# Kernel optimization log

Measured on AMD Instinct MI355X. Metric: run time of the kernel, lower is better.

Reference implementation:

```python
import jax, jax.numpy as jnp
import numpy as np

EMB, HEADS = 1024, 16
B, T = 4, 1024

def setup_inputs() -> dict:
    key = jax.random.key(0)
    ks = jax.random.split(key, 6)
    sc = 1.0 / np.sqrt(EMB)
    return {
        "x": jax.random.normal(ks[0], (B, T, EMB), jnp.float32),
        "Wq": jax.random.normal(ks[1], (EMB, EMB), jnp.float32) * sc,
        "Wk": jax.random.normal(ks[2], (EMB, EMB), jnp.float32) * sc,
        "Wv": jax.random.normal(ks[3], (EMB, EMB), jnp.float32) * sc,
        "Wo": jax.random.normal(ks[4], (EMB, EMB), jnp.float32) * sc,
        "bo": jnp.zeros((EMB,), jnp.float32),
    }

def reference(x, Wq, Wk, Wv, Wo, bo):
    b, t, e = x.shape
    h = HEADS
    s = e // h
    # nn.Linear(emb, emb, bias=False): y = x @ W.T
    q = (x @ Wq.T).reshape(b, t, h, s).transpose(0, 2, 1, 3)  # (b,h,t,s)
    k = (x @ Wk.T).reshape(b, t, h, s).transpose(0, 2, 1, 3)
    v = (x @ Wv.T).reshape(b, t, h, s).transpose(0, 2, 1, 3)
    scale = e ** 0.25  # original scales q and k each by emb**(1/4)
    q = q / scale
    k = k / scale
    dot = jnp.einsum('bhqs,bhks->bhqk', q, k)  # (b,h,t,t)
    # causal mask: strict upper triangle -> -inf (mask_diagonal=False)
    causal = jnp.tril(jnp.ones((t, t), dtype=bool))
    dot = jnp.where(causal[None, None], dot, -jnp.inf)
    attn = jax.nn.softmax(dot, axis=-1)
    out = jnp.einsum('bhqk,bhks->bhqs', attn, v)  # (b,h,t,s)
    out = out.transpose(0, 2, 1, 3).reshape(b, t, e)
    return out @ Wo.T + bo
```

## Files before the change

### kernel.cpp

```cpp
#include <hip/hip_runtime.h>
#include <hip/hip_bf16.h>
#include <stdint.h>


typedef __attribute__((ext_vector_type(8))) short short8;
typedef __attribute__((ext_vector_type(4))) float f32x4;
typedef __attribute__((ext_vector_type(16))) float f32x16;

__device__ __forceinline__ unsigned short f2bf(float f) {
    union { float f; unsigned int u; } v; v.f = f;
    unsigned int r = v.u + 0x7FFFu + ((v.u >> 16) & 1u);
    return (unsigned short)(r >> 16);
}
__device__ __forceinline__ unsigned short f2bf_trunc(float f) {
    union { float f; unsigned int u; } v; v.f = f;
    return (unsigned short)(v.u >> 16);
}

__device__ __forceinline__ void gload_lds16(const ushort* g, ushort* l) {
    __builtin_amdgcn_global_load_lds(
        (const __attribute__((address_space(1))) void*)g,
        (__attribute__((address_space(3))) void*)l,
        16, 0, 0);
}

__device__ __forceinline__ void wait_vmcnt_0() { asm volatile("s_waitcnt vmcnt(0)" ::: "memory"); }
__device__ __forceinline__ void wait_vmcnt_3() { asm volatile("s_waitcnt vmcnt(3)" ::: "memory"); }
__device__ __forceinline__ void wait_vmcnt_4() { asm volatile("s_waitcnt vmcnt(4)" ::: "memory"); }

__device__ __forceinline__ void block_barrier() {
    __builtin_amdgcn_sched_barrier(0);
    __builtin_amdgcn_s_barrier();
    __builtin_amdgcn_sched_barrier(0);
}
__device__ __forceinline__ void lgk0() {
    asm volatile("s_waitcnt lgkmcnt(0)" ::: "memory");
    __builtin_amdgcn_sched_barrier(0);
}

__global__ __launch_bounds__(256) void cast_bf16(
    const float* __restrict__ x,  const float* __restrict__ wq,
    const float* __restrict__ wk, const float* __restrict__ wv,
    const float* __restrict__ wo, ushort* __restrict__ dst)
{
    size_t e0 = (size_t)(blockIdx.x * 256 + threadIdx.x) * 4;
    const float* src; size_t off;
    if      (e0 < 4194304u) { src = x;  off = e0; }
    else if (e0 < 5242880u) { src = wq; off = e0 - 4194304u; }
    else if (e0 < 6291456u) { src = wk; off = e0 - 5242880u; }
    else if (e0 < 7340032u) { src = wv; off = e0 - 6291456u; }
    else                    { src = wo; off = e0 - 7340032u; }
    float4 v = *(const float4*)(src + off);
    ushort4 o;
    o.x = f2bf(v.x); o.y = f2bf(v.y); o.z = f2bf(v.z); o.w = f2bf(v.w);
    *(ushort4*)(dst + e0) = o;
}

__global__ __launch_bounds__(512) void gemm_qkv_8ph(
    const ushort* __restrict__ A, const ushort* __restrict__ B,
    ushort* __restrict__ Qb, ushort* __restrict__ Kb, ushort* __restrict__ Vtb)
{
    __shared__ ushort lds[2][2][2][128 * 64];

    const int id = blockIdx.x;
    const int swz = (id & 7) * 24 + (id >> 3);
    const int bx = swz % 12, by = swz / 12;
    const int n0 = bx * 256, m0 = by * 256;
    const int t = threadIdx.x, w = t >> 6, l = t & 63;
    const int l15 = l & 15, l4 = l >> 4;
    const int wr = w >> 2, wc = w & 3;
    const int K = 1024;

    auto stage_half = [&](const ushort* gsrc, ushort* dst) {
        #pragma unroll
        for (int i = 0; i < 2; ++i) {
            int slot = i * 512 + t;
            int r = slot >> 3, blk = slot & 7;
            gload_lds16(gsrc + (size_t)r * K + ((blk ^ (r & 7)) << 3),
                        dst + (i * 512 + w * 64) * 8);
        }
    };
    auto stageA = [&](int kt, int h, int buf) {
        stage_half(A + (size_t)(m0 + h * 128) * K + kt * 64, &lds[buf][0][h][0]);
    };
    auto stageB = [&](int kt, int h, int buf) {
        stage_half(B + (size_t)(n0 + h * 128) * K + kt * 64, &lds[buf][1][h][0]);
    };

    short8 af[8];
    short8 vb0[4], vb1[4];
    f32x4 acc[8][4] = {};

    auto readA = [&](int buf, int qm) {
        const ushort* base = &lds[buf][0][wr][0];
        #pragma unroll
        for (int kk = 0; kk < 2; ++kk)
            #pragma unroll
            for (int mt = 0; mt < 4; ++mt) {
                int row = qm * 64 + mt * 16 + l15;
                af[kk * 4 + mt] = *(const short8*)
                    &base[row * 64 + (((kk * 4 + l4) ^ (row & 7)) << 3)];
            }
    };
    auto readB0 = [&](int buf, int qn) {
        const ushort* base = &lds[buf][1][wc >> 1][0];
        #pragma unroll
        for (int kk = 0; kk < 2; ++kk)
            #pragma unroll
            for (int nt = 0; nt < 2; ++nt) {
                int row = (wc & 1) * 64 + qn * 32 + nt * 16 + l15;
                vb0[kk * 2 + nt] = *(const short8*)
                    &base[row * 64 + (((kk * 4 + l4) ^ (row & 7)) << 3)];
            }
    };
    auto readB1 = [&](int buf, int qn) {
        const ushort* base = &lds[buf][1][wc >> 1][0];
        #pragma unroll
        for (int kk = 0; kk < 2; ++kk)
            #pragma unroll
            for (int nt = 0; nt < 2; ++nt) {
                int row = (wc & 1) * 64 + qn * 32 + nt * 16 + l15;
                vb1[kk * 2 + nt] = *(const short8*)
                    &base[row * 64 + (((kk * 4 + l4) ^ (row & 7)) << 3)];
            }
    };
    auto mfma_vb0 = [&](int qm, int qn) {
        __builtin_amdgcn_s_setprio(1);
        #pragma unroll
        for (int kk = 0; kk < 2; ++kk)
            #pragma unroll
            for (int mt = 0; mt < 4; ++mt)
                #pragma unroll
                for (int nt = 0; nt < 2; ++nt)
                    acc[qm * 4 + mt][qn * 2 + nt] =
                        __builtin_amdgcn_mfma_f32_16x16x32_bf16(
                            af[kk * 4 + mt], vb0[kk * 2 + nt],
                            acc[qm * 4 + mt][qn * 2 + nt], 0, 0, 0);
        __builtin_amdgcn_s_setprio(0);
    };
    auto mfma_vb1 = [&](int qm, int qn) {
        __builtin_amdgcn_s_setprio(1);
        #pragma unroll
        for (int kk = 0; kk < 2; ++kk)
            #pragma unroll
            for (int mt = 0; mt < 4; ++mt)
                #pragma unroll
                for (int nt = 0; nt < 2; ++nt)
                    acc[qm * 4 + mt][qn * 2 + nt] =
                        __builtin_amdgcn_mfma_f32_16x16x32_bf16(
                            af[kk * 4 + mt], vb1[kk * 2 + nt],
                            acc[qm * 4 + mt][qn * 2 + nt], 0, 0, 0);
        __builtin_amdgcn_s_setprio(0);
    };

    stageB(0, 0, 0); stageB(0, 1, 0); stageA(0, 0, 0); stageA(0, 1, 0);
    stageB(1, 0, 1); stageB(1, 1, 1);
    wait_vmcnt_4();
    block_barrier();

    for (int j = 0; j < 8; ++j) {
        const bool more = (j < 7);
        readA(0, 0); readB0(0, 0);
        stageA(2 * j + 1, 0, 1);
        block_barrier(); lgk0();
        mfma_vb0(0, 0);
        block_barrier();
        readB1(0, 1);
        stageA(2 * j + 1, 1, 1);
        block_barrier(); lgk0();
        mfma_vb1(0, 1);
        block_barrier();
        readA(0, 1);
        if (more) stageB(2 * j + 2, 0, 0);
        block_barrier(); lgk0();
        mfma_vb1(1, 1);
        block_barrier();
        if (more) stageB(2 * j + 2, 1, 0);
        block_barrier(); lgk0();
        mfma_vb0(1, 0);
        if (more) wait_vmcnt_4(); else wait_vmcnt_0();
        block_barrier();
        readA(1, 0); readB0(1, 0);
        if (more) stageA(2 * j + 2, 0, 0);
        block_barrier(); lgk0();
        mfma_vb0(0, 0);
        block_barrier();
        readB1(1, 1);
        if (more) stageA(2 * j + 2, 1, 0);
        block_barrier(); lgk0();
        mfma_vb1(0, 1);
        block_barrier();
        readA(1, 1);
        if (more) stageB(2 * j + 3, 0, 1);
        block_barrier(); lgk0();
        mfma_vb1(1, 1);
        block_barrier();
        if (more) stageB(2 * j + 3, 1, 1);
        block_barrier(); lgk0();
        mfma_vb0(1, 0);
        if (more) { wait_vmcnt_4(); block_barrier(); }
    }

    #pragma unroll
    for (int qm = 0; qm < 2; ++qm) {
        #pragma unroll
        for (int mt = 0; mt < 4; ++mt) {
            int row = m0 + wr * 128 + qm * 64 + mt * 16 + l4 * 4;
            int b = row >> 10, tq = row & 1023;
            #pragma unroll
            for (int qn = 0; qn < 2; ++qn) {
                #pragma unroll
                for (int nt = 0; nt < 2; ++nt) {
                    int col = n0 + wc * 64 + qn * 32 + nt * 16 + l15;
                    int sel = col >> 10;
                    int cw  = col & 1023;
                    int h = cw >> 6, s = cw & 63;
                    f32x4 v = acc[qm * 4 + mt][qn * 2 + nt];
                    if (sel == 2) {
                        ushort4 o;
                        o.x = f2bf(v[0]); o.y = f2bf(v[1]);
                        o.z = f2bf(v[2]); o.w = f2bf(v[3]);
                        *(ushort4*)&Vtb[(((size_t)(b * 16 + h)) * 64 + s) * 1024 + tq] = o;
                    } else {
                        ushort* dst = (sel == 0) ? Qb : Kb;
                        float scl = (sel == 0) ? 0.03125f : 1.0f;
                        #pragma unroll
                        for (int jj = 0; jj < 4; ++jj)
                            dst[(((size_t)(b * 16 + h)) * 1024 + tq + jj) * 64 + s] =
                                f2bf(v[jj] * scl);
                    }
                }
            }
        }
    }
}

template<int MODE, int BM, int WRg, int WCg>
__global__ __launch_bounds__(256) void gemm_bt(
    const ushort* __restrict__ A, const ushort* __restrict__ B,
    float* __restrict__ Cout, const float* __restrict__ bias)
{
    constexpr int MF = BM / (32 * WRg);
    constexpr int NF = 128 / (32 * WCg);
    constexpr int NSTEP = 32;
    const int K = 1024;
    const int n0 = blockIdx.x * 128;
    const int m0 = blockIdx.y * BM;
    const int t  = threadIdx.x;
    const int w  = t >> 6, l = t & 63;
    const int l31 = l & 31, lh = l >> 5;
    const int wr = w / WCg, wc = w % WCg;

    __shared__ ushort As[3 * BM * 32];
    __shared__ ushort Bs[3 * 128 * 32];

    auto stage = [&](int j) {
        const int buf = j % 3;
        const int k0 = j * 32;
        #pragma unroll
        for (int i = 0; i < BM / 64; ++i) {
            int slot = i * 256 + t;
            int r = slot >> 2, blk = slot & 3;
            gload_lds16(A + (size_t)(m0 + r) * K + k0 + ((blk ^ ((r >> 1) & 3)) << 3),
                        &As[buf * BM * 32 + (i * 256 + w * 64) * 8]);
        }
        #pragma unroll
        for (int i = 0; i < 2; ++i) {
            int slot = i * 256 + t;
            int r = slot >> 2, blk = slot & 3;
            gload_lds16(B + (size_t)(n0 + r) * K + k0 + ((blk ^ ((r >> 1) & 3)) << 3),
                        &Bs[buf * 128 * 32 + (i * 256 + w * 64) * 8]);
        }
    };

    f32x16 acc[MF][NF] = {};

    stage(0); stage(1);
    for (int kt = 0; kt < NSTEP; ++kt) {
        if (kt < NSTEP - 1) { if (BM == 128) wait_vmcnt_4(); else wait_vmcnt_3(); }
        else wait_vmcnt_0();
        block_barrier();
        if (kt + 2 < NSTEP) stage(kt + 2);

        const ushort* Ab = &As[(kt % 3) * BM * 32];
        const ushort* Bb = &Bs[(kt % 3) * 128 * 32];
        #pragma unroll
        for (int kk = 0; kk < 2; ++kk) {
            const int c = kk * 2 + lh;
            short8 af[MF], bf[NF];
            #pragma unroll
            for (int mt = 0; mt < MF; ++mt) {
                int row = wr * (MF * 32) + mt * 32 + l31;
                af[mt] = *(const short8*)&Ab[row * 32 + ((c ^ ((row >> 1) & 3)) << 3)];
            }
            #pragma unroll
            for (int nt = 0; nt < NF; ++nt) {
                int row = wc * (NF * 32) + nt * 32 + l31;
                bf[nt] = *(const short8*)&Bs[(kt % 3) * 128 * 32 + row * 32 + ((c ^ ((row >> 1) & 3)) << 3)];
            }
            #pragma unroll
            for (int mt = 0; mt < MF; ++mt)
                #pragma unroll
                for (int nt = 0; nt < NF; ++nt)
                    acc[mt][nt] = __builtin_amdgcn_mfma_f32_32x32x16_bf16(
                        af[mt], bf[nt], acc[mt][nt], 0, 0, 0);
        }
    }

    #pragma unroll
    for (int mt = 0; mt < MF; ++mt) {
        int rbase = m0 + wr * (MF * 32) + mt * 32 + 4 * lh;
        #pragma unroll
        for (int nt = 0; nt < NF; ++nt) {
            int col = n0 + wc * (NF * 32) + nt * 32 + l31;
            float bi = bias[col];
            #pragma unroll
            for (int reg = 0; reg < 16; ++reg) {
                int row = rbase + (reg & 3) + 8 * (reg >> 2);
                Cout[(size_t)row * 1024 + col] = acc[mt][nt][reg] + bi;
            }
        }
    }
}

__global__ __launch_bounds__(64) void attn_kernel(
    const ushort* __restrict__ Q, const ushort* __restrict__ Kp,
    const ushort* __restrict__ Vt, ushort* __restrict__ O)
{
    __shared__ ushort Ps[32 * 64];
    const int id = blockIdx.x;
    const int bh = id & 63;
    const int g  = 31 - (id >> 6);
    const int l = threadIdx.x;
    const int l15 = l & 15, l4 = l >> 4;

    const ushort* Qbase = Q  + ((size_t)bh * 1024 + (size_t)g * 32) * 64;
    const ushort* Kbase = Kp + (size_t)bh * 1024 * 64;
    const ushort* Vtb   = Vt + (size_t)bh * 64 * 1024;

    short8 qa[2][2];
    #pragma unroll
    for (int kk = 0; kk < 2; ++kk)
        #pragma unroll
        for (int mt = 0; mt < 2; ++mt)
            qa[kk][mt] = *(const short8*)(Qbase + (size_t)(mt * 16 + l15) * 64 + (kk * 4 + l4) * 8);

    float l_acc[8];
    #pragma unroll
    for (int i = 0; i < 8; ++i) l_acc[i] = 0.f;
    f32x4 accO[2][4] = {};

    const int qmin = g * 32;
    const int nkv = (g >> 1) + 1;
    for (int kvt = 0; kvt < nkv; ++kvt) {
        short8 kb[2][4];
        #pragma unroll
        for (int kk = 0; kk < 2; ++kk)
            #pragma unroll
            for (int nt = 0; nt < 4; ++nt)
                kb[kk][nt] = *(const short8*)
                    (Kbase + (size_t)(kvt * 64 + nt * 16 + l15) * 64 + (kk * 4 + l4) * 8);
        short8 vb[2][4];
        #pragma unroll
        for (int kk = 0; kk < 2; ++kk)
            #pragma unroll
            for (int st = 0; st < 4; ++st)
                vb[kk][st] = *(const short8*)
                    (Vtb + (size_t)(st * 16 + l15) * 1024 + kvt * 64 + (kk * 4 + l4) * 8);

        f32x4 sf[2][4] = {};
        #pragma unroll
        for (int kk = 0; kk < 2; ++kk)
            #pragma unroll
            for (int mt = 0; mt < 2; ++mt)
                #pragma unroll
                for (int nt = 0; nt < 4; ++nt)
                    sf[mt][nt] = __builtin_amdgcn_mfma_f32_16x16x32_bf16(
                        qa[kk][mt], kb[kk][nt], sf[mt][nt], 0, 0, 0);

        const bool domask = (kvt * 64 + 63 > qmin);
        #pragma unroll
        for (int mt = 0; mt < 2; ++mt) {
            #pragma unroll
            for (int r = 0; r < 4; ++r) {
                const int qrow = qmin + mt * 16 + l4 * 4 + r;
                const int qlocal = mt * 16 + l4 * 4 + r;
                const int idx = mt * 4 + r;
                #pragma unroll
                for (int nt = 0; nt < 4; ++nt) {
                    int col = kvt * 64 + nt * 16 + l15;
                    float p = (domask && col > qrow) ? 0.f : __expf(sf[mt][nt][r]);
                    l_acc[idx] += p;
                    int c = nt * 16 + l15;
                    Ps[qlocal * 64 + (((c >> 3) ^ (qlocal & 7)) << 3) + (c & 7)] =
                        f2bf_trunc(p);
                }
            }
        }
        lgk0();

        #pragma unroll
        for (int kk = 0; kk < 2; ++kk) {
            short8 pa[2];
            #pragma unroll
            for (int mt = 0; mt < 2; ++mt) {
                int row = mt * 16 + l15;
                pa[mt] = *(const short8*)&Ps[row * 64 + (((kk * 4 + l4) ^ (row & 7)) << 3)];
            }
            #pragma unroll
            for (int mt = 0; mt < 2; ++mt)
                #pragma unroll
                for (int st = 0; st < 4; ++st)
                    accO[mt][st] = __builtin_amdgcn_mfma_f32_16x16x32_bf16(
                        pa[mt], vb[kk][st], accO[mt][st], 0, 0, 0);
        }
    }

    const int b = bh >> 4, h = bh & 15;
    #pragma unroll
    for (int mt = 0; mt < 2; ++mt) {
        #pragma unroll
        for (int r = 0; r < 4; ++r) {
            float s = l_acc[mt * 4 + r];
            s += __shfl_xor(s, 1);
            s += __shfl_xor(s, 2);
            s += __shfl_xor(s, 4);
            s += __shfl_xor(s, 8);
            float inv = 1.0f / s;
            int tq = qmin + mt * 16 + l4 * 4 + r;
            #pragma unroll
            for (int st = 0; st < 4; ++st) {
                int sc = st * 16 + l15;
                O[((size_t)b * 1024 + tq) * 1024 + h * 64 + sc] =
                    f2bf(accO[mt][st][r] * inv);
            }
        }
    }
}

extern "C" void kernel_launch(void* const* d_in, const int* in_sizes, int n_in,
                              void* d_out, int out_size, void* d_ws, size_t ws_size,
                              hipStream_t stream) {
    const float* x  = (const float*)d_in[0];
    const float* wq = (const float*)d_in[1];
    const float* wk = (const float*)d_in[2];
    const float* wv = (const float*)d_in[3];
    const float* wo = (const float*)d_in[4];
    const float* bo = (const float*)d_in[5];
    float* out = (float*)d_out;

    ushort* ws  = (ushort*)d_ws;
    ushort* xb  = ws;
    ushort* wb  = ws + (4u << 20);
    ushort* Qb  = ws + (8u << 20);
    ushort* Kb  = ws + (12u << 20);
    ushort* Vtb = ws + (16u << 20);
    ushort* Ob  = ws + (20u << 20);

    cast_bf16<<<8192, 256, 0, stream>>>(x, wq, wk, wv, wo, ws);
    gemm_qkv_8ph<<<192, 512, 0, stream>>>(xb, wb, Qb, Kb, Vtb);
    attn_kernel<<<2048, 64, 0, stream>>>(Qb, Kb, Vtb, Ob);
    gemm_bt<1, 64, 1, 4><<<dim3(8, 64), 256, 0, stream>>>(
        Ob, wb + (3u << 20), out, bo);
}
```

Baseline: 106.1 us.

## Split attention KV loop across two wavefronts and combine partial results in LDS

The attention kernel now runs two wavefronts per block. Each wavefront processes half of the causal KV tiles for the same 32-query tile, and wave 1's partial output and row sums are reduced into wave 0 through shared memory. No running max is kept, so the two partials can be added directly. This is a split-K flash-decoding style change meant to shorten the per-block critical path and raise parallelism. In exchange it adds LDS usage (about 8KB plus 2×4KB), a block barrier and a combine step. It also includes a trivial cleanup that reuses the Bb pointer in the GEMM.

```diff
diff --git a/kernel.cpp b/kernel.cpp
--- a/kernel.cpp
+++ b/kernel.cpp
@@ -296,7 +296,7 @@
             #pragma unroll
             for (int nt = 0; nt < NF; ++nt) {
                 int row = wc * (NF * 32) + nt * 32 + l31;
-                bf[nt] = *(const short8*)&Bs[(kt % 3) * 128 * 32 + row * 32 + ((c ^ ((row >> 1) & 3)) << 3)];
+                bf[nt] = *(const short8*)&Bb[row * 32 + ((c ^ ((row >> 1) & 3)) << 3)];
             }
             #pragma unroll
             for (int mt = 0; mt < MF; ++mt)
@@ -323,15 +323,18 @@
     }
 }
 
-__global__ __launch_bounds__(64) void attn_kernel(
+__global__ __launch_bounds__(128) void attn_kernel(
     const ushort* __restrict__ Q, const ushort* __restrict__ Kp,
     const ushort* __restrict__ Vt, ushort* __restrict__ O)
 {
-    __shared__ ushort Ps[32 * 64];
+    __shared__ ushort Ps[2][32 * 64];
+    __shared__ float cmb[32 * 64];
+    __shared__ float lcmb[32];
+
     const int id = blockIdx.x;
     const int bh = id & 63;
     const int g  = 31 - (id >> 6);
-    const int l = threadIdx.x;
+    const int t = threadIdx.x, w = t >> 6, l = t & 63;
     const int l15 = l & 15, l4 = l >> 4;
 
     const ushort* Qbase = Q  + ((size_t)bh * 1024 + (size_t)g * 32) * 64;
@@ -352,15 +355,18 @@
 
     const int qmin = g * 32;
     const int nkv = (g >> 1) + 1;
-    for (int kvt = 0; kvt < nkv; ++kvt) {
-        short8 kb[2][4];
+    const int h = (nkv + 1) >> 1;
+    const int kv_lo = w ? h : 0;
+    const int kv_hi = w ? nkv : h;
+
+    for (int kvt = kv_lo; kvt < kv_hi; ++kvt) {
+        short8 kb[2][4], vb[2][4];
         #pragma unroll
         for (int kk = 0; kk < 2; ++kk)
             #pragma unroll
             for (int nt = 0; nt < 4; ++nt)
                 kb[kk][nt] = *(const short8*)
                     (Kbase + (size_t)(kvt * 64 + nt * 16 + l15) * 64 + (kk * 4 + l4) * 8);
-        short8 vb[2][4];
         #pragma unroll
         for (int kk = 0; kk < 2; ++kk)
             #pragma unroll
@@ -392,7 +398,7 @@
                     float p = (domask && col > qrow) ? 0.f : __expf(sf[mt][nt][r]);
                     l_acc[idx] += p;
                     int c = nt * 16 + l15;
-                    Ps[qlocal * 64 + (((c >> 3) ^ (qlocal & 7)) << 3) + (c & 7)] =
+                    Ps[w][qlocal * 64 + (((c >> 3) ^ (qlocal & 7)) << 3) + (c & 7)] =
                         f2bf_trunc(p);
                 }
             }
@@ -405,7 +411,7 @@
             #pragma unroll
             for (int mt = 0; mt < 2; ++mt) {
                 int row = mt * 16 + l15;
-                pa[mt] = *(const short8*)&Ps[row * 64 + (((kk * 4 + l4) ^ (row & 7)) << 3)];
+                pa[mt] = *(const short8*)&Ps[w][row * 64 + (((kk * 4 + l4) ^ (row & 7)) << 3)];
             }
             #pragma unroll
             for (int mt = 0; mt < 2; ++mt)
@@ -416,23 +422,47 @@
         }
     }
 
-    const int b = bh >> 4, h = bh & 15;
+    float lred[8];
     #pragma unroll
-    for (int mt = 0; mt < 2; ++mt) {
-        #pragma unroll
-        for (int r = 0; r < 4; ++r) {
-            float s = l_acc[mt * 4 + r];
-            s += __shfl_xor(s, 1);
-            s += __shfl_xor(s, 2);
-            s += __shfl_xor(s, 4);
-            s += __shfl_xor(s, 8);
-            float inv = 1.0f / s;
-            int tq = qmin + mt * 16 + l4 * 4 + r;
-            #pragma unroll
-            for (int st = 0; st < 4; ++st) {
-                int sc = st * 16 + l15;
-                O[((size_t)b * 1024 + tq) * 1024 + h * 64 + sc] =
-                    f2bf(accO[mt][st][r] * inv);
+    for (int i = 0; i < 8; ++i) {
+        float s = l_acc[i];
+        s += __shfl_xor(s, 1);
+        s += __shfl_xor(s, 2);
+        s += __shfl_xor(s, 4);
+        s += __shfl_xor(s, 8);
+        lred[i] = s;
+    }
+
+    if (w == 1) {
+        #pragma unroll
+        for (int mt = 0; mt < 2; ++mt) {
+            #pragma unroll
+            for (int r = 0; r < 4; ++r) {
+                int row = mt * 16 + l4 * 4 + r;
+                if (l15 == 0) lcmb[row] = lred[mt * 4 + r];
+                #pragma unroll
+                for (int st = 0; st < 4; ++st)
+                    cmb[row * 64 + st * 16 + l15] = accO[mt][st][r];
+            }
+        }
+    }
+    __syncthreads();
+    if (w == 0) {
+        const int b = bh >> 4, hh = bh & 15;
+        #pragma unroll
+        for (int mt = 0; mt < 2; ++mt) {
+            #pragma unroll
+            for (int r = 0; r < 4; ++r) {
+                int row = mt * 16 + l4 * 4 + r;
+                float s = lred[mt * 4 + r] + lcmb[row];
+                float inv = 1.0f / s;
+                int tq = qmin + row;
+                #pragma unroll
+                for (int st = 0; st < 4; ++st) {
+                    int sc = st * 16 + l15;
+                    float o = accO[mt][st][r] + cmb[row * 64 + sc];
+                    O[((size_t)b * 1024 + tq) * 1024 + hh * 64 + sc] = f2bf(o * inv);
+                }
             }
         }
     }
@@ -459,7 +489,7 @@
 
     cast_bf16<<<8192, 256, 0, stream>>>(x, wq, wk, wv, wo, ws);
     gemm_qkv_8ph<<<192, 512, 0, stream>>>(xb, wb, Qb, Kb, Vtb);
-    attn_kernel<<<2048, 64, 0, stream>>>(Qb, Kb, Vtb, Ob);
+    attn_kernel<<<2048, 128, 0, stream>>>(Qb, Kb, Vtb, Ob);
     gemm_bt<1, 64, 1, 4><<<dim3(8, 64), 256, 0, stream>>>(
         Ob, wb + (3u << 20), out, bo);
 }
```

Result: no change. 105.3 us (-0.7%).

## Keep attention probabilities in registers via transposed 32x32 MFMA and permlane swap

Applied to the files above, without the earlier changes.

The attention kernel now computes S^T = K·Q^T with 32x32x16 MFMAs, so each lane holds the scores for one query row. The probabilities are packed to bf16 with v_cvt_pk_bf16_f32 and rearranged with v_permlane32_swap into the A-operand layout for the PV MFMA. This removes the LDS round trip and the wait on it, and it also simplifies the row-sum reduction. The causal tail is peeled out so masking and the upper half-tile are done only where needed, at the cost of higher register pressure and reliance on gfx950-specific instructions.

```diff
diff --git a/kernel.cpp b/kernel.cpp
--- a/kernel.cpp
+++ b/kernel.cpp
@@ -11,10 +11,6 @@
     union { float f; unsigned int u; } v; v.f = f;
     unsigned int r = v.u + 0x7FFFu + ((v.u >> 16) & 1u);
     return (unsigned short)(r >> 16);
-}
-__device__ __forceinline__ unsigned short f2bf_trunc(float f) {
-    union { float f; unsigned int u; } v; v.f = f;
-    return (unsigned short)(v.u >> 16);
 }
 
 __device__ __forceinline__ void gload_lds16(const ushort* g, ushort* l) {
@@ -36,6 +32,15 @@
 __device__ __forceinline__ void lgk0() {
     asm volatile("s_waitcnt lgkmcnt(0)" ::: "memory");
     __builtin_amdgcn_sched_barrier(0);
+}
+
+__device__ __forceinline__ unsigned int cvtpk(float lo, float hi) {
+    unsigned int r;
+    asm("v_cvt_pk_bf16_f32 %0, %1, %2" : "=v"(r) : "v"(lo), "v"(hi));
+    return r;
+}
+__device__ __forceinline__ void plswap(unsigned int& x, unsigned int& y) {
+    asm volatile("v_permlane32_swap_b32 %0, %1" : "+v"(x), "+v"(y));
 }
 
 __global__ __launch_bounds__(256) void cast_bf16(
@@ -296,7 +301,7 @@
             #pragma unroll
             for (int nt = 0; nt < NF; ++nt) {
                 int row = wc * (NF * 32) + nt * 32 + l31;
-                bf[nt] = *(const short8*)&Bs[(kt % 3) * 128 * 32 + row * 32 + ((c ^ ((row >> 1) & 3)) << 3)];
+                bf[nt] = *(const short8*)&Bb[row * 32 + ((c ^ ((row >> 1) & 3)) << 3)];
             }
             #pragma unroll
             for (int mt = 0; mt < MF; ++mt)
@@ -327,114 +332,126 @@
     const ushort* __restrict__ Q, const ushort* __restrict__ Kp,
     const ushort* __restrict__ Vt, ushort* __restrict__ O)
 {
-    __shared__ ushort Ps[32 * 64];
     const int id = blockIdx.x;
     const int bh = id & 63;
     const int g  = 31 - (id >> 6);
     const int l = threadIdx.x;
-    const int l15 = l & 15, l4 = l >> 4;
+    const int l31 = l & 31, hi = l >> 5;
 
     const ushort* Qbase = Q  + ((size_t)bh * 1024 + (size_t)g * 32) * 64;
     const ushort* Kbase = Kp + (size_t)bh * 1024 * 64;
     const ushort* Vtb   = Vt + (size_t)bh * 64 * 1024;
 
-    short8 qa[2][2];
+    short8 qb[4];
     #pragma unroll
-    for (int kk = 0; kk < 2; ++kk)
-        #pragma unroll
-        for (int mt = 0; mt < 2; ++mt)
-            qa[kk][mt] = *(const short8*)(Qbase + (size_t)(mt * 16 + l15) * 64 + (kk * 4 + l4) * 8);
-
-    float l_acc[8];
-    #pragma unroll
-    for (int i = 0; i < 8; ++i) l_acc[i] = 0.f;
-    f32x4 accO[2][4] = {};
-
-    const int qmin = g * 32;
+    for (int ks = 0; ks < 4; ++ks)
+        qb[ks] = *(const short8*)(Qbase + (size_t)l31 * 64 + ks * 16 + hi * 8);
+
+    f32x16 accO0 = {}, accO1 = {};
+    float lsum = 0.f;
+    const int qrow = g * 32 + l31;
     const int nkv = (g >> 1) + 1;
-    for (int kvt = 0; kvt < nkv; ++kvt) {
-        short8 kb[2][4];
-        #pragma unroll
-        for (int kk = 0; kk < 2; ++kk)
-            #pragma unroll
-            for (int nt = 0; nt < 4; ++nt)
-                kb[kk][nt] = *(const short8*)
-                    (Kbase + (size_t)(kvt * 64 + nt * 16 + l15) * 64 + (kk * 4 + l4) * 8);
-        short8 vb[2][4];
-        #pragma unroll
-        for (int kk = 0; kk < 2; ++kk)
-            #pragma unroll
-            for (int st = 0; st < 4; ++st)
-                vb[kk][st] = *(const short8*)
-                    (Vtb + (size_t)(st * 16 + l15) * 1024 + kvt * 64 + (kk * 4 + l4) * 8);
-
-        f32x4 sf[2][4] = {};
-        #pragma unroll
-        for (int kk = 0; kk < 2; ++kk)
-            #pragma unroll
-            for (int mt = 0; mt < 2; ++mt)
-                #pragma unroll
-                for (int nt = 0; nt < 4; ++nt)
-                    sf[mt][nt] = __builtin_amdgcn_mfma_f32_16x16x32_bf16(
-                        qa[kk][mt], kb[kk][nt], sf[mt][nt], 0, 0, 0);
-
-        const bool domask = (kvt * 64 + 63 > qmin);
-        #pragma unroll
-        for (int mt = 0; mt < 2; ++mt) {
-            #pragma unroll
-            for (int r = 0; r < 4; ++r) {
-                const int qrow = qmin + mt * 16 + l4 * 4 + r;
-                const int qlocal = mt * 16 + l4 * 4 + r;
-                const int idx = mt * 4 + r;
-                #pragma unroll
-                for (int nt = 0; nt < 4; ++nt) {
-                    int col = kvt * 64 + nt * 16 + l15;
-                    float p = (domask && col > qrow) ? 0.f : __expf(sf[mt][nt][r]);
-                    l_acc[idx] += p;
-                    int c = nt * 16 + l15;
-                    Ps[qlocal * 64 + (((c >> 3) ^ (qlocal & 7)) << 3) + (c & 7)] =
-                        f2bf_trunc(p);
-                }
-            }
-        }
-        lgk0();
-
-        #pragma unroll
-        for (int kk = 0; kk < 2; ++kk) {
-            short8 pa[2];
-            #pragma unroll
-            for (int mt = 0; mt < 2; ++mt) {
-                int row = mt * 16 + l15;
-                pa[mt] = *(const short8*)&Ps[row * 64 + (((kk * 4 + l4) ^ (row & 7)) << 3)];
-            }
-            #pragma unroll
-            for (int mt = 0; mt < 2; ++mt)
-                #pragma unroll
-                for (int st = 0; st < 4; ++st)
-                    accO[mt][st] = __builtin_amdgcn_mfma_f32_16x16x32_bf16(
-                        pa[mt], vb[kk][st], accO[mt][st], 0, 0, 0);
-        }
-    }
-
+
+    auto pv_ks = [&](const float* pf, int ks, const short8* vb0p, const short8* vb1p) {
+        const int r0 = (ks & 1) * 8;
+        unsigned int A0 = cvtpk(pf[r0 + 0], pf[r0 + 1]);
+        unsigned int A1 = cvtpk(pf[r0 + 2], pf[r0 + 3]);
+        unsigned int B0 = cvtpk(pf[r0 + 4], pf[r0 + 5]);
+        unsigned int B1 = cvtpk(pf[r0 + 6], pf[r0 + 7]);
+        plswap(A0, B0);
+        plswap(A1, B1);
+        union { unsigned int u[4]; short8 s; } pa;
+        pa.u[0] = A0; pa.u[1] = A1; pa.u[2] = B0; pa.u[3] = B1;
+        accO0 = __builtin_amdgcn_mfma_f32_32x32x16_bf16(pa.s, vb0p[ks], accO0, 0, 0, 0);
+        accO1 = __builtin_amdgcn_mfma_f32_32x32x16_bf16(pa.s, vb1p[ks], accO1, 0, 0, 0);
+    };
+
+    for (int kvt = 0; kvt < nkv - 1; ++kvt) {
+        short8 ka0[4], ka1[4], vb0[4], vb1[4];
+        #pragma unroll
+        for (int ks = 0; ks < 4; ++ks) {
+            ka0[ks] = *(const short8*)(Kbase + (size_t)(kvt * 64 + l31) * 64 + ks * 16 + hi * 8);
+            ka1[ks] = *(const short8*)(Kbase + (size_t)(kvt * 64 + 32 + l31) * 64 + ks * 16 + hi * 8);
+        }
+        #pragma unroll
+        for (int ks = 0; ks < 4; ++ks) {
+            vb0[ks] = *(const short8*)(Vtb + (size_t)l31 * 1024 + kvt * 64 + ks * 16 + hi * 8);
+            vb1[ks] = *(const short8*)(Vtb + (size_t)(32 + l31) * 1024 + kvt * 64 + ks * 16 + hi * 8);
+        }
+        f32x16 sf0 = {}, sf1 = {};
+        #pragma unroll
+        for (int ks = 0; ks < 4; ++ks) {
+            sf0 = __builtin_amdgcn_mfma_f32_32x32x16_bf16(ka0[ks], qb[ks], sf0, 0, 0, 0);
+            sf1 = __builtin_amdgcn_mfma_f32_32x32x16_bf16(ka1[ks], qb[ks], sf1, 0, 0, 0);
+        }
+        float p[32];
+        #pragma unroll
+        for (int r = 0; r < 16; ++r) { p[r]      = __expf(sf0[r]); lsum += p[r]; }
+        #pragma unroll
+        for (int r = 0; r < 16; ++r) { p[16 + r] = __expf(sf1[r]); lsum += p[16 + r]; }
+        pv_ks(p,      0, vb0, vb1);
+        pv_ks(p,      1, vb0, vb1);
+        pv_ks(p + 16, 2, vb0, vb1);
+        pv_ks(p + 16, 3, vb0, vb1);
+    }
+
+    {
+        const int kvt = nkv - 1;
+        const int kvb = kvt * 64;
+        short8 ka0[4], vb0[4], vb1[4];
+        #pragma unroll
+        for (int ks = 0; ks < 4; ++ks)
+            ka0[ks] = *(const short8*)(Kbase + (size_t)(kvb + l31) * 64 + ks * 16 + hi * 8);
+        #pragma unroll
+        for (int ks = 0; ks < 4; ++ks) {
+            vb0[ks] = *(const short8*)(Vtb + (size_t)l31 * 1024 + kvb + ks * 16 + hi * 8);
+            vb1[ks] = *(const short8*)(Vtb + (size_t)(32 + l31) * 1024 + kvb + ks * 16 + hi * 8);
+        }
+        f32x16 sf0 = {};
+        #pragma unroll
+        for (int ks = 0; ks < 4; ++ks)
+            sf0 = __builtin_amdgcn_mfma_f32_32x32x16_bf16(ka0[ks], qb[ks], sf0, 0, 0, 0);
+
+        float p[32];
+        #pragma unroll
+        for (int r = 0; r < 16; ++r) {
+            int kv = kvb + (r & 3) + 8 * (r >> 2) + 4 * hi;
+            float pr = (kv > qrow) ? 0.f : __expf(sf0[r]);
+            p[r] = pr; lsum += pr;
+        }
+        pv_ks(p, 0, vb0, vb1);
+        pv_ks(p, 1, vb0, vb1);
+
+        if (g & 1) {
+            short8 ka1[4];
+            #pragma unroll
+            for (int ks = 0; ks < 4; ++ks)
+                ka1[ks] = *(const short8*)(Kbase + (size_t)(kvb + 32 + l31) * 64 + ks * 16 + hi * 8);
+            f32x16 sf1 = {};
+            #pragma unroll
+            for (int ks = 0; ks < 4; ++ks)
+                sf1 = __builtin_amdgcn_mfma_f32_32x32x16_bf16(ka1[ks], qb[ks], sf1, 0, 0, 0);
+            #pragma unroll
+            for (int r = 0; r < 16; ++r) {
+                int kv = kvb + 32 + (r & 3) + 8 * (r >> 2) + 4 * hi;
+                float pr = (kv > qrow) ? 0.f : __expf(sf1[r]);
+                p[16 + r] = pr; lsum += pr;
+            }
+            pv_ks(p + 16, 2, vb0, vb1);
+            pv_ks(p + 16, 3, vb0, vb1);
+        }
+    }
+
+    float ltot = lsum + __shfl_xor(lsum, 32);
+    float inv = 1.0f / ltot;
     const int b = bh >> 4, h = bh & 15;
     #pragma unroll
-    for (int mt = 0; mt < 2; ++mt) {
-        #pragma unroll
-        for (int r = 0; r < 4; ++r) {
-            float s = l_acc[mt * 4 + r];
-            s += __shfl_xor(s, 1);
-            s += __shfl_xor(s, 2);
-            s += __shfl_xor(s, 4);
-            s += __shfl_xor(s, 8);
-            float inv = 1.0f / s;
-            int tq = qmin + mt * 16 + l4 * 4 + r;
-            #pragma unroll
-            for (int st = 0; st < 4; ++st) {
-                int sc = st * 16 + l15;
-                O[((size_t)b * 1024 + tq) * 1024 + h * 64 + sc] =
-                    f2bf(accO[mt][st][r] * inv);
-            }
-        }
+    for (int r = 0; r < 16; ++r) {
+        int qr = (r & 3) + 8 * (r >> 2) + 4 * hi;
+        float invr = __shfl(inv, qr);
+        int tq = g * 32 + qr;
+        O[((size_t)b * 1024 + tq) * 1024 + h * 64 + l31]      = f2bf(accO0[r] * invr);
+        O[((size_t)b * 1024 + tq) * 1024 + h * 64 + 32 + l31] = f2bf(accO1[r] * invr);
     }
 }
 
```

Measured after the change: 104.3 us. About the same (-1.7%).
